# Performance work log

Hardware: AMD Instinct MI355X
Metric: run time of the kernel (lower is better)

## Reference

```python
import jax, jax.numpy as jnp
import numpy as np

B, L, D, H, NL, V, W = 4, 2048, 512, 8, 4, 258, 8
HD = D // H


def setup_inputs() -> dict:
    key = jax.random.key(0)
    ks = jax.random.split(key, 12)
    s = 0.02
    x = jax.random.randint(ks[0], (B, L), 0, V, dtype=jnp.int32)
    patch_lengths = jnp.full((B, 256), W, dtype=jnp.int32)  # sum over patches == L
    emb = jax.random.normal(ks[1], (V, D), jnp.float32) * s
    ent_w = jax.random.normal(ks[2], (D, 1), jnp.float32) * s
    ent_b = jnp.zeros((D,), jnp.float32)
    qkv_w = jax.random.normal(ks[3], (NL, 3 * D, D), jnp.float32) * s
    qkv_b = jnp.zeros((NL, 3 * D), jnp.float32)
    ao_w = jax.random.normal(ks[4], (NL, D, D), jnp.float32) * s
    ao_b = jnp.zeros((NL, D), jnp.float32)
    ln1_s = jnp.ones((NL, D), jnp.float32)
    ln1_b = jnp.zeros((NL, D), jnp.float32)
    ln2_s = jnp.ones((NL, D), jnp.float32)
    ln2_b = jnp.zeros((NL, D), jnp.float32)
    ff1_w = jax.random.normal(ks[5], (NL, 4 * D, D), jnp.float32) * s
    ff1_b = jnp.zeros((NL, 4 * D), jnp.float32)
    ff2_w = jax.random.normal(ks[6], (NL, D, 4 * D), jnp.float32) * s
    ff2_b = jnp.zeros((NL, D), jnp.float32)
    out_w = jax.random.normal(ks[7], (V, D), jnp.float32) * s
    return {"emb": emb, "ent_w": ent_w, "ent_b": ent_b, "qkv_w": qkv_w,
            "qkv_b": qkv_b, "ao_w": ao_w, "ao_b": ao_b, "ln1_s": ln1_s,
            "ln1_b": ln1_b, "ln2_s": ln2_s, "ln2_b": ln2_b, "ff1_w": ff1_w,
            "ff1_b": ff1_b, "ff2_w": ff2_w, "ff2_b": ff2_b, "out_w": out_w,
            "x": x, "patch_lengths": patch_lengths}


def _layernorm(h, scale, bias, eps=1e-5):
    mu = jnp.mean(h, axis=-1, keepdims=True)
    var = jnp.mean(jnp.square(h - mu), axis=-1, keepdims=True)
    return (h - mu) * jax.lax.rsqrt(var + eps) * scale + bias


def _entropy_features(x, dtype):
    # fused sliding-window histogram via one-hot cumsum (replaces per-window bincount loop)
    onehot = jax.nn.one_hot(x, 256, dtype=dtype)            # [B, L, 256]
    c = jnp.cumsum(onehot, axis=1)
    cpad = jnp.concatenate([jnp.zeros_like(c[:, :1]), c], axis=1)
    counts = cpad[:, W:] - cpad[:, :-W]                     # [B, L-W+1, 256]
    p = counts / W
    ent = -jnp.sum(p * jnp.log2(p + 1e-10), axis=-1)        # zero-count terms contribute exactly 0
    full = jnp.zeros(x.shape, dtype).at[:, :x.shape[1] - W + 1].set(ent)
    return full[..., None]                                  # [B, L, 1]


def _block(h, p):
    qkv_w, qkv_b, ao_w, ao_b, l1s, l1b, l2s, l2b, f1w, f1b, f2w, f2b = p
    g = _layernorm(h, l1s, l1b)
    qkv = g @ qkv_w.T + qkv_b                                # [B, L, 3D]
    q, k, v = jnp.split(qkv, 3, axis=-1)
    q = q.reshape(B, L, H, HD)
    k = k.reshape(B, L, H, HD)
    v = v.reshape(B, L, H, HD)
    scores = jnp.einsum('blhd,bmhd->bhlm', q, k) / np.sqrt(HD).astype(h.dtype)
    attn = jax.nn.softmax(scores, axis=-1)
    o = jnp.einsum('bhlm,bmhd->blhd', attn, v).reshape(B, L, D)
    h = h + o @ ao_w.T + ao_b
    g = _layernorm(h, l2s, l2b)
    g = jax.nn.gelu(g @ f1w.T + f1b, approximate=False) @ f2w.T + f2b
    return h + g, None


def reference(emb, ent_w, ent_b, qkv_w, qkv_b, ao_w, ao_b, ln1_s, ln1_b,
              ln2_s, ln2_b, ff1_w, ff1_b, ff2_w, ff2_b, out_w, x, patch_lengths):
    tok = emb[x]                                             # [B, L, D]
    ent = _entropy_features(x, tok.dtype)                    # [B, L, 1]
    ent_emb = ent * ent_w[:, 0] + ent_b                      # Linear(1, D)
    h = tok + ent_emb
    h, _ = jax.lax.scan(_block, h,
                        (qkv_w, qkv_b, ao_w, ao_b, ln1_s, ln1_b,
                         ln2_s, ln2_b, ff1_w, ff1_b, ff2_w, ff2_b))
    # NOTE: the original module's global_transformer/patch-pool branch does not
    # feed the returned logits (dead code); logits come from the local stream h.
    logits = h @ out_w.T                                     # [B, L, V]
    return logits
```

## Files before the change

### kernel.cpp

```cpp
#include <hip/hip_runtime.h>
#include <hip/hip_bf16.h>
#include <math.h>

#define BB 4
#define LL 2048
#define DD 512
#define HH 8
#define NLAYER 4
#define VV 258
#define WW 8
#define HDIM 64
#define MM (BB * LL)
#define VPAD 384

typedef __attribute__((ext_vector_type(8))) short short8v;
typedef __attribute__((ext_vector_type(4))) float float4v;

typedef __attribute__((address_space(3))) unsigned int lds_u32;
typedef const __attribute__((address_space(1))) unsigned int glb_u32;

__device__ __forceinline__ unsigned short f2bf(float x) {
    unsigned int u = __float_as_uint(x);
    unsigned int r = (u + 0x7fffu + ((u >> 16) & 1u)) >> 16;
    return (unsigned short)r;
}

__device__ __forceinline__ unsigned lds_addr(const void* p) {
    return (unsigned)(size_t)(__attribute__((address_space(3))) const void*)p;
}

__global__ __launch_bounds__(256)
void cvt_kernel(const float* __restrict__ in, unsigned short* __restrict__ out, int n)
{
    int i = (blockIdx.x * 256 + threadIdx.x) * 4;
    if (i < n) {
        float4 v = *reinterpret_cast<const float4*>(in + i);
        uint2 pk;
        pk.x = (unsigned)f2bf(v.x) | ((unsigned)f2bf(v.y) << 16);
        pk.y = (unsigned)f2bf(v.z) | ((unsigned)f2bf(v.w) << 16);
        *reinterpret_cast<uint2*>(out + i) = pk;
    }
}

__global__ __launch_bounds__(256)
void cvt_pad_kernel(const float* __restrict__ in, unsigned short* __restrict__ out)
{
    int i = blockIdx.x * 256 + threadIdx.x;
    int row = i >> 9;
    out[i] = (row < VV) ? f2bf(in[i]) : (unsigned short)0;
}

__global__ __launch_bounds__(256)
void embed_ent_kernel(const int* __restrict__ x,
                      const float* __restrict__ emb,
                      const float* __restrict__ ent_w,
                      const float* __restrict__ ent_b,
                      float* __restrict__ h)
{
    int row = blockIdx.x;
    int b = row / LL, l = row % LL;

    float ent = 0.f;
    if (l <= LL - WW) {
        int win[WW];
        #pragma unroll
        for (int i = 0; i < WW; i++) win[i] = x[b * LL + l + i];
        float s = 0.f;
        #pragma unroll
        for (int i = 0; i < WW; i++) {
            if (win[i] < 256) {
                int c = 0;
                #pragma unroll
                for (int j = 0; j < WW; j++) c += (win[j] == win[i]) ? 1 : 0;
                s += log2f((float)c * 0.125f + 1e-10f);
            }
        }
        ent = -s * 0.125f;
    }

    int tok = x[b * LL + l];
    const float* erow = emb + (size_t)tok * DD;
    float* hrow = h + (size_t)row * DD;
    for (int d = threadIdx.x; d < DD; d += blockDim.x) {
        hrow[d] = erow[d] + ent * ent_w[d] + ent_b[d];
    }
}

__global__ __launch_bounds__(256)
void ln_kernel(const float* __restrict__ h,
               const float* __restrict__ scale,
               const float* __restrict__ bias,
               unsigned short* __restrict__ g)
{
    int w = threadIdx.x >> 6, lane = threadIdx.x & 63;
    int row = blockIdx.x * 4 + w;
    const float* hr = h + (size_t)row * DD + lane * 8;

    float v[8];
    *reinterpret_cast<float4*>(v)     = *reinterpret_cast<const float4*>(hr);
    *reinterpret_cast<float4*>(v + 4) = *reinterpret_cast<const float4*>(hr + 4);

    float sum = 0.f, sq = 0.f;
    #pragma unroll
    for (int i = 0; i < 8; i++) { sum += v[i]; sq += v[i] * v[i]; }
    #pragma unroll
    for (int off = 32; off > 0; off >>= 1) {
        sum += __shfl_xor(sum, off);
        sq  += __shfl_xor(sq, off);
    }
    float mu = sum * (1.f / DD);
    float var = sq * (1.f / DD) - mu * mu;
    float rstd = rsqrtf(var + 1e-5f);

    float s[8], bi[8];
    *reinterpret_cast<float4*>(s)      = *reinterpret_cast<const float4*>(scale + lane * 8);
    *reinterpret_cast<float4*>(s + 4)  = *reinterpret_cast<const float4*>(scale + lane * 8 + 4);
    *reinterpret_cast<float4*>(bi)     = *reinterpret_cast<const float4*>(bias + lane * 8);
    *reinterpret_cast<float4*>(bi + 4) = *reinterpret_cast<const float4*>(bias + lane * 8 + 4);

    unsigned int pk[4];
    #pragma unroll
    for (int i = 0; i < 4; i++) {
        unsigned short lo = f2bf((v[2*i]   - mu) * rstd * s[2*i]   + bi[2*i]);
        unsigned short hi = f2bf((v[2*i+1] - mu) * rstd * s[2*i+1] + bi[2*i+1]);
        pk[i] = (unsigned)lo | ((unsigned)hi << 16);
    }
    *reinterpret_cast<uint4*>(g + (size_t)row * DD + lane * 8) =
        *reinterpret_cast<const uint4*>(pk);
}

template<bool HAS_BIAS, bool GELU, bool RESID, bool OUT_BF16>
__global__ __launch_bounds__(256)
void gemm_mfma(const unsigned short* __restrict__ A,
               const unsigned short* __restrict__ W,
               const float* __restrict__ bias,
               const float* __restrict__ resid,
               void* __restrict__ Cv,
               int Nn, int Kk)
{
    __shared__ unsigned short As[2][128 * 64];
    __shared__ unsigned short Bs[2][128 * 64];

    int t = threadIdx.x;
    int w = t >> 6, lane = t & 63;
    int wr = w >> 1, wc = w & 1;
    int l15 = lane & 15, l4 = lane >> 4;
    int m0 = blockIdx.y * 128, n0 = blockIdx.x * 128;

    int lrow = lane >> 3;
    int segp = (lane & 7) ^ lrow;

    float4v acc[4][4];
    #pragma unroll
    for (int i = 0; i < 4; i++)
        #pragma unroll
        for (int j = 0; j < 4; j++)
            acc[i][j] = (float4v){0.f, 0.f, 0.f, 0.f};

    #define STAGE(buf, k0) do {                                                   \
        _Pragma("unroll")                                                         \
        for (int i_ = 0; i_ < 4; i_++) {                                          \
            int r_ = i_ * 32 + w * 8 + lrow;                                      \
            __builtin_amdgcn_global_load_lds(                                     \
                (glb_u32*)(A + (size_t)(m0 + r_) * Kk + (k0) + segp * 8),         \
                (lds_u32*)(As[buf] + i_ * 2048 + w * 512), 16, 0, 0);             \
            __builtin_amdgcn_global_load_lds(                                     \
                (glb_u32*)(W + (size_t)(n0 + r_) * Kk + (k0) + segp * 8),         \
                (lds_u32*)(Bs[buf] + i_ * 2048 + w * 512), 16, 0, 0);             \
        } } while (0)

    int nk = Kk >> 6;
    STAGE(0, 0);
    for (int kt = 0; kt < nk; kt++) {
        int cur = kt & 1;
        if (kt + 1 < nk) {
            STAGE(cur ^ 1, (kt + 1) << 6);
            __builtin_amdgcn_sched_barrier(0);
            asm volatile("s_waitcnt vmcnt(8)");
            __builtin_amdgcn_sched_barrier(0);
        } else {
            __builtin_amdgcn_sched_barrier(0);
            asm volatile("s_waitcnt vmcnt(0)");
            __builtin_amdgcn_sched_barrier(0);
        }
        __builtin_amdgcn_s_barrier();

        const char* asb = (const char*)As[cur];
        const char* bsb = (const char*)Bs[cur];
        #pragma unroll
        for (int kc = 0; kc < 2; kc++) {
            short8v af[4], bfr[4];
            #pragma unroll
            for (int mf = 0; mf < 4; mf++) {
                int row = wr * 64 + mf * 16 + l15;
                int off = (row * 128 + kc * 64 + l4 * 16) ^ ((row & 7) << 4);
                af[mf] = *reinterpret_cast<const short8v*>(asb + off);
            }
            #pragma unroll
            for (int nf = 0; nf < 4; nf++) {
                int row = wc * 64 + nf * 16 + l15;
                int off = (row * 128 + kc * 64 + l4 * 16) ^ ((row & 7) << 4);
                bfr[nf] = *reinterpret_cast<const short8v*>(bsb + off);
            }
            #pragma unroll
            for (int mf = 0; mf < 4; mf++)
                #pragma unroll
                for (int nf = 0; nf < 4; nf++)
                    acc[mf][nf] = __builtin_amdgcn_mfma_f32_16x16x32_bf16(
                        af[mf], bfr[nf], acc[mf][nf], 0, 0, 0);
        }
        __builtin_amdgcn_s_barrier();
    }
    #undef STAGE

    #pragma unroll
    for (int mf = 0; mf < 4; mf++)
        #pragma unroll
        for (int nf = 0; nf < 4; nf++)
            #pragma unroll
            for (int r = 0; r < 4; r++) {
                int m = m0 + wr * 64 + mf * 16 + l4 * 4 + r;
                int n = n0 + wc * 64 + nf * 16 + l15;
                if (n < Nn) {
                    float v = acc[mf][nf][r];
                    if (HAS_BIAS) v += bias[n];
                    if (GELU)     v = 0.5f * v * (1.f + erff(v * 0.70710678118654752f));
                    if (RESID)    v += resid[(size_t)m * Nn + n];
                    if (OUT_BF16) ((unsigned short*)Cv)[(size_t)m * Nn + n] = f2bf(v);
                    else          ((float*)Cv)[(size_t)m * Nn + n] = v;
                }
            }
}

__global__ __launch_bounds__(512, 4)
void attn_mfma(const unsigned short* __restrict__ qkv, unsigned short* __restrict__ o)
{
    __shared__ unsigned short Kl[64 * 64];
    __shared__ unsigned short Vs[64 * 64];
    __shared__ unsigned short Pl[8 * 16 * 64];
    __shared__ float Scl[8][16];

    int t = threadIdx.x, w = t >> 6, lane = t & 63;
    int l15 = lane & 15, l4 = lane >> 4;

    int flat = blockIdx.x;
    int swz = (flat & 7) * 64 + (flat >> 3);
    int qt = swz & 15, hh = (swz >> 4) & 7, b = swz >> 7;

    int q0 = qt * 128 + w * 16;
    const int RS = 3 * DD;

    short8v qf[2];
    #pragma unroll
    for (int dh = 0; dh < 2; dh++) {
        size_t addr = (size_t)(b * LL + q0 + l15) * RS + hh * HDIM + dh * 32 + l4 * 8;
        qf[dh] = *reinterpret_cast<const short8v*>(qkv + addr);
    }

    float4v o_acc[4];
    #pragma unroll
    for (int dt = 0; dt < 4; dt++) o_acc[dt] = (float4v){0.f, 0.f, 0.f, 0.f};
    float m_run = -1e30f, l_run = 0.f;

    char* pbase = (char*)Pl + w * 2048;

    int krow = t >> 3, kseg = t & 7;
    int vrow = ((t >> 5) << 2) | ((t >> 1) & 3);
    int vseg = (((t >> 3) & 3) << 1) | (t & 1);

    unsigned vbase = lds_addr(Vs) + ((lane >> 4) << 10)
                   + (((lane >> 2) & 3) << 5) + ((lane & 3) << 3);

    for (int kb = 0; kb < LL / 64; kb++) {
        size_t gaK = (size_t)(b * LL + kb * 64 + krow) * RS + hh * HDIM + DD + kseg * 8;
        size_t gaV = (size_t)(b * LL + kb * 64 + vrow) * RS + hh * HDIM + 2 * DD + vseg * 8;
        short8v krg = *reinterpret_cast<const short8v*>(qkv + gaK);
        short8v vrg = *reinterpret_cast<const short8v*>(qkv + gaV);
        __syncthreads();
        {
            int koff = (krow * 128 + kseg * 16) ^ ((krow & 7) << 4);
            *reinterpret_cast<short8v*>((char*)Kl + koff) = krg;
            *reinterpret_cast<short8v*>((char*)Vs + t * 16) = vrg;
        }
        __syncthreads();

        float4v s_acc[4];
        __builtin_amdgcn_s_setprio(1);
        #pragma unroll
        for (int nt = 0; nt < 4; nt++) {
            s_acc[nt] = (float4v){0.f, 0.f, 0.f, 0.f};
            #pragma unroll
            for (int dh = 0; dh < 2; dh++) {
                int row = nt * 16 + l15;
                int off = (row * 128 + dh * 64 + l4 * 16) ^ ((row & 7) << 4);
                short8v kf = *reinterpret_cast<const short8v*>((const char*)Kl + off);
                s_acc[nt] = __builtin_amdgcn_mfma_f32_16x16x32_bf16(kf, qf[dh], s_acc[nt], 0, 0, 0);
            }
        }
        __builtin_amdgcn_s_setprio(0);

        float mm = -1e30f;
        #pragma unroll
        for (int nt = 0; nt < 4; nt++)
            #pragma unroll
            for (int r = 0; r < 4; r++)
                mm = fmaxf(mm, s_acc[nt][r]);
        mm *= 0.125f;
        mm = fmaxf(mm, __shfl_xor(mm, 16));
        mm = fmaxf(mm, __shfl_xor(mm, 32));

        if (!__all(mm <= m_run + 8.f)) {
            float mnew = fmaxf(m_run, mm);
            float sc = __expf(m_run - mnew);
            m_run = mnew;
            l_run *= sc;
            if (l4 == 0) Scl[w][l15] = sc;
            float4 scv = *reinterpret_cast<const float4*>(&Scl[w][l4 * 4]);
            #pragma unroll
            for (int dt = 0; dt < 4; dt++) {
                o_acc[dt][0] *= scv.x; o_acc[dt][1] *= scv.y;
                o_acc[dt][2] *= scv.z; o_acc[dt][3] *= scv.w;
            }
        }

        float ps = 0.f;
        #pragma unroll
        for (int nt = 0; nt < 4; nt++) {
            float p0 = __expf(fmaf(s_acc[nt][0], 0.125f, -m_run));
            float p1 = __expf(fmaf(s_acc[nt][1], 0.125f, -m_run));
            float p2 = __expf(fmaf(s_acc[nt][2], 0.125f, -m_run));
            float p3 = __expf(fmaf(s_acc[nt][3], 0.125f, -m_run));
            ps += (p0 + p1) + (p2 + p3);
            unsigned int pk0, pk1;
            asm("v_cvt_pk_bf16_f32 %0, %1, %2" : "=v"(pk0) : "v"(p0), "v"(p1));
            asm("v_cvt_pk_bf16_f32 %0, %1, %2" : "=v"(pk1) : "v"(p2), "v"(p3));
            uint2 pk; pk.x = pk0; pk.y = pk1;
            int off = (l15 * 128 + nt * 32 + l4 * 8) ^ ((l15 & 7) << 4);
            *reinterpret_cast<uint2*>(pbase + off) = pk;
        }
        l_run += ps;

        #pragma unroll
        for (int kc = 0; kc < 2; kc++) {
            int poff = (l15 * 128 + kc * 64 + l4 * 16) ^ ((l15 & 7) << 4);
            short8v pf = *reinterpret_cast<const short8v*>(pbase + poff);
            unsigned long long tr0, tr1, tr2, tr3, tr4, tr5, tr6, tr7;
            unsigned ab = vbase + kc * 4096;
            asm volatile("ds_read_b64_tr_b16 %0, %1" : "=v"(tr0) : "v"(ab));
            asm volatile("ds_read_b64_tr_b16 %0, %1" : "=v"(tr1) : "v"(ab + 512));
            asm volatile("ds_read_b64_tr_b16 %0, %1" : "=v"(tr2) : "v"(ab + 128));
            asm volatile("ds_read_b64_tr_b16 %0, %1" : "=v"(tr3) : "v"(ab + 640));
            asm volatile("ds_read_b64_tr_b16 %0, %1" : "=v"(tr4) : "v"(ab + 256));
            asm volatile("ds_read_b64_tr_b16 %0, %1" : "=v"(tr5) : "v"(ab + 768));
            asm volatile("ds_read_b64_tr_b16 %0, %1" : "=v"(tr6) : "v"(ab + 384));
            asm volatile("ds_read_b64_tr_b16 %0, %1" : "=v"(tr7) : "v"(ab + 896));
            asm volatile("s_waitcnt lgkmcnt(0)");
            __builtin_amdgcn_sched_barrier(0);
            __builtin_amdgcn_s_setprio(1);
            union { unsigned long long q[2]; short8v v; } u0, u1, u2, u3;
            u0.q[0] = tr0; u0.q[1] = tr1;
            u1.q[0] = tr2; u1.q[1] = tr3;
            u2.q[0] = tr4; u2.q[1] = tr5;
            u3.q[0] = tr6; u3.q[1] = tr7;
            o_acc[0] = __builtin_amdgcn_mfma_f32_16x16x32_bf16(pf, u0.v, o_acc[0], 0, 0, 0);
            o_acc[1] = __builtin_amdgcn_mfma_f32_16x16x32_bf16(pf, u1.v, o_acc[1], 0, 0, 0);
            o_acc[2] = __builtin_amdgcn_mfma_f32_16x16x32_bf16(pf, u2.v, o_acc[2], 0, 0, 0);
            o_acc[3] = __builtin_amdgcn_mfma_f32_16x16x32_bf16(pf, u3.v, o_acc[3], 0, 0, 0);
            __builtin_amdgcn_s_setprio(0);
        }
    }

    float lt = l_run;
    lt += __shfl_xor(lt, 16);
    lt += __shfl_xor(lt, 32);
    if (l4 == 0) Scl[w][l15] = 1.f / lt;
    float4 iv = *reinterpret_cast<const float4*>(&Scl[w][l4 * 4]);
    float invs[4] = {iv.x, iv.y, iv.z, iv.w};
    #pragma unroll
    for (int r = 0; r < 4; r++) {
        int qg = q0 + l4 * 4 + r;
        #pragma unroll
        for (int dt = 0; dt < 4; dt++) {
            o[(size_t)(b * LL + qg) * DD + hh * HDIM + dt * 16 + l15] =
                f2bf(o_acc[dt][r] * invs[r]);
        }
    }
}

extern "C" void kernel_launch(void* const* d_in, const int* in_sizes, int n_in,
                              void* d_out, int out_size, void* d_ws, size_t ws_size,
                              hipStream_t stream)
{
    const float* emb    = (const float*)d_in[0];
    const float* ent_w  = (const float*)d_in[1];
    const float* ent_b  = (const float*)d_in[2];
    const float* qkv_w  = (const float*)d_in[3];
    const float* qkv_b  = (const float*)d_in[4];
    const float* ao_w   = (const float*)d_in[5];
    const float* ao_b   = (const float*)d_in[6];
    const float* ln1_s  = (const float*)d_in[7];
    const float* ln1_b  = (const float*)d_in[8];
    const float* ln2_s  = (const float*)d_in[9];
    const float* ln2_b  = (const float*)d_in[10];
    const float* ff1_w  = (const float*)d_in[11];
    const float* ff1_b  = (const float*)d_in[12];
    const float* ff2_w  = (const float*)d_in[13];
    const float* ff2_b  = (const float*)d_in[14];
    const float* out_w  = (const float*)d_in[15];
    const int*   x      = (const int*)d_in[16];

    float* out = (float*)d_out;

    const int NQW = NLAYER * 3 * DD * DD;
    const int NAW = NLAYER * DD * DD;
    const int NF1 = NLAYER * 4 * DD * DD;
    const int NF2 = NLAYER * DD * 4 * DD;

    char* p = (char*)d_ws;
    unsigned short* wq  = (unsigned short*)p; p += (size_t)NQW * 2;
    unsigned short* wa  = (unsigned short*)p; p += (size_t)NAW * 2;
    unsigned short* w1  = (unsigned short*)p; p += (size_t)NF1 * 2;
    unsigned short* w2  = (unsigned short*)p; p += (size_t)NF2 * 2;
    unsigned short* wob = (unsigned short*)p; p += (size_t)VPAD * DD * 2;
    float*          h   = (float*)p;          p += (size_t)MM * DD * 4;
    unsigned short* hb  = (unsigned short*)p; p += (size_t)MM * DD * 2;
    unsigned short* gb  = (unsigned short*)p; p += (size_t)MM * DD * 2;
    unsigned short* ob  = (unsigned short*)p; p += (size_t)MM * DD * 2;
    unsigned short* bb  = (unsigned short*)p; p += (size_t)MM * 4 * DD * 2;

    dim3 blk(256);

    cvt_kernel<<<NQW / 1024, blk, 0, stream>>>(qkv_w, wq, NQW);
    cvt_kernel<<<NAW / 1024, blk, 0, stream>>>(ao_w,  wa, NAW);
    cvt_kernel<<<NF1 / 1024, blk, 0, stream>>>(ff1_w, w1, NF1);
    cvt_kernel<<<NF2 / 1024, blk, 0, stream>>>(ff2_w, w2, NF2);
    cvt_pad_kernel<<<(VPAD * DD) / 256, blk, 0, stream>>>(out_w, wob);

    embed_ent_kernel<<<MM, blk, 0, stream>>>(x, emb, ent_w, ent_b, h);

    for (int layer = 0; layer < NLAYER; layer++) {
        const unsigned short* qw = wq + (size_t)layer * 3 * DD * DD;
        const unsigned short* aw = wa + (size_t)layer * DD * DD;
        const unsigned short* f1 = w1 + (size_t)layer * 4 * DD * DD;
        const unsigned short* f2 = w2 + (size_t)layer * DD * 4 * DD;
        const float* qb  = qkv_b + (size_t)layer * 3 * DD;
        const float* ab  = ao_b  + (size_t)layer * DD;
        const float* l1s = ln1_s + (size_t)layer * DD;
        const float* l1b = ln1_b + (size_t)layer * DD;
        const float* l2s = ln2_s + (size_t)layer * DD;
        const float* l2b = ln2_b + (size_t)layer * DD;
        const float* f1b = ff1_b + (size_t)layer * 4 * DD;
        const float* f2b = ff2_b + (size_t)layer * DD;

        ln_kernel<<<MM / 4, blk, 0, stream>>>(h, l1s, l1b, gb);

        {
            dim3 grid((3 * DD) / 128, MM / 128);
            gemm_mfma<true, false, false, true><<<grid, blk, 0, stream>>>(
                gb, qw, qb, nullptr, bb, 3 * DD, DD);
        }

        attn_mfma<<<512, 512, 0, stream>>>(bb, ob);

        {
            dim3 grid(DD / 128, MM / 128);
            gemm_mfma<true, false, true, false><<<grid, blk, 0, stream>>>(
                ob, aw, ab, h, h, DD, DD);
        }

        ln_kernel<<<MM / 4, blk, 0, stream>>>(h, l2s, l2b, gb);

        {
            dim3 grid((4 * DD) / 128, MM / 128);
            gemm_mfma<true, true, false, true><<<grid, blk, 0, stream>>>(
                gb, f1, f1b, nullptr, bb, 4 * DD, DD);
        }

        {
            dim3 grid(DD / 128, MM / 128);
            gemm_mfma<true, false, true, false><<<grid, blk, 0, stream>>>(
                bb, f2, f2b, h, h, DD, 4 * DD);
        }
    }

    cvt_kernel<<<(MM * DD) / 1024, blk, 0, stream>>>(h, hb, MM * DD);
    {
        dim3 grid(VPAD / 128, MM / 128);
        gemm_mfma<false, false, false, false><<<grid, blk, 0, stream>>>(
            hb, wob, nullptr, nullptr, out, VV, DD);
    }
}
```

Baseline: 800.7 us.

## Double-buffer attention K/V tiles and fuse embed+LN and final bf16 cast

Attention now double-buffers K/V in LDS, prefetching the next tile into registers while computing on the current one. This leaves one barrier per iteration instead of two, and launch bounds drop to 2 blocks per SM to fit the extra LDS. The embedding kernel is fused with the first layernorm, and the last FF2 GEMM also writes a bf16 copy of h. Together these remove one LN launch and the final conversion pass, at the cost of lower occupancy in attention.

```diff
diff --git a/kernel.cpp b/kernel.cpp
--- a/kernel.cpp
+++ b/kernel.cpp
@@ -51,13 +51,17 @@
 }
 
 __global__ __launch_bounds__(256)
-void embed_ent_kernel(const int* __restrict__ x,
-                      const float* __restrict__ emb,
-                      const float* __restrict__ ent_w,
-                      const float* __restrict__ ent_b,
-                      float* __restrict__ h)
-{
-    int row = blockIdx.x;
+void embed_ln_kernel(const int* __restrict__ x,
+                     const float* __restrict__ emb,
+                     const float* __restrict__ ent_w,
+                     const float* __restrict__ ent_b,
+                     const float* __restrict__ ln_s,
+                     const float* __restrict__ ln_b,
+                     float* __restrict__ h,
+                     unsigned short* __restrict__ g)
+{
+    int w = threadIdx.x >> 6, lane = threadIdx.x & 63;
+    int row = blockIdx.x * 4 + w;
     int b = row / LL, l = row % LL;
 
     float ent = 0.f;
@@ -78,12 +82,50 @@
         ent = -s * 0.125f;
     }
 
-    int tok = x[b * LL + l];
-    const float* erow = emb + (size_t)tok * DD;
-    float* hrow = h + (size_t)row * DD;
-    for (int d = threadIdx.x; d < DD; d += blockDim.x) {
-        hrow[d] = erow[d] + ent * ent_w[d] + ent_b[d];
-    }
+    int tok = x[row];
+    const float* erow = emb + (size_t)tok * DD + lane * 8;
+    float v[8], ew[8], eb[8];
+    *reinterpret_cast<float4*>(v)      = *reinterpret_cast<const float4*>(erow);
+    *reinterpret_cast<float4*>(v + 4)  = *reinterpret_cast<const float4*>(erow + 4);
+    *reinterpret_cast<float4*>(ew)     = *reinterpret_cast<const float4*>(ent_w + lane * 8);
+    *reinterpret_cast<float4*>(ew + 4) = *reinterpret_cast<const float4*>(ent_w + lane * 8 + 4);
+    *reinterpret_cast<float4*>(eb)     = *reinterpret_cast<const float4*>(ent_b + lane * 8);
+    *reinterpret_cast<float4*>(eb + 4) = *reinterpret_cast<const float4*>(ent_b + lane * 8 + 4);
+
+    float sum = 0.f, sq = 0.f;
+    #pragma unroll
+    for (int i = 0; i < 8; i++) {
+        v[i] = v[i] + ent * ew[i] + eb[i];
+        sum += v[i]; sq += v[i] * v[i];
+    }
+    float* hr = h + (size_t)row * DD + lane * 8;
+    *reinterpret_cast<float4*>(hr)     = *reinterpret_cast<const float4*>(v);
+    *reinterpret_cast<float4*>(hr + 4) = *reinterpret_cast<const float4*>(v + 4);
+
+    #pragma unroll
+    for (int off = 32; off > 0; off >>= 1) {
+        sum += __shfl_xor(sum, off);
+        sq  += __shfl_xor(sq, off);
+    }
+    float mu = sum * (1.f / DD);
+    float var = sq * (1.f / DD) - mu * mu;
+    float rstd = rsqrtf(var + 1e-5f);
+
+    float s8[8], bi[8];
+    *reinterpret_cast<float4*>(s8)     = *reinterpret_cast<const float4*>(ln_s + lane * 8);
+    *reinterpret_cast<float4*>(s8 + 4) = *reinterpret_cast<const float4*>(ln_s + lane * 8 + 4);
+    *reinterpret_cast<float4*>(bi)     = *reinterpret_cast<const float4*>(ln_b + lane * 8);
+    *reinterpret_cast<float4*>(bi + 4) = *reinterpret_cast<const float4*>(ln_b + lane * 8 + 4);
+
+    unsigned int pk[4];
+    #pragma unroll
+    for (int i = 0; i < 4; i++) {
+        unsigned short lo = f2bf((v[2*i]   - mu) * rstd * s8[2*i]   + bi[2*i]);
+        unsigned short hi = f2bf((v[2*i+1] - mu) * rstd * s8[2*i+1] + bi[2*i+1]);
+        pk[i] = (unsigned)lo | ((unsigned)hi << 16);
+    }
+    *reinterpret_cast<uint4*>(g + (size_t)row * DD + lane * 8) =
+        *reinterpret_cast<const uint4*>(pk);
 }
 
 __global__ __launch_bounds__(256)
@@ -129,13 +171,14 @@
         *reinterpret_cast<const uint4*>(pk);
 }
 
-template<bool HAS_BIAS, bool GELU, bool RESID, bool OUT_BF16>
+template<bool HAS_BIAS, bool GELU, bool RESID, int OMODE>
 __global__ __launch_bounds__(256)
 void gemm_mfma(const unsigned short* __restrict__ A,
                const unsigned short* __restrict__ W,
                const float* __restrict__ bias,
                const float* __restrict__ resid,
                void* __restrict__ Cv,
+               unsigned short* __restrict__ Cb,
                int Nn, int Kk)
 {
     __shared__ unsigned short As[2][128 * 64];
@@ -226,17 +269,21 @@
                     if (HAS_BIAS) v += bias[n];
                     if (GELU)     v = 0.5f * v * (1.f + erff(v * 0.70710678118654752f));
                     if (RESID)    v += resid[(size_t)m * Nn + n];
-                    if (OUT_BF16) ((unsigned short*)Cv)[(size_t)m * Nn + n] = f2bf(v);
-                    else          ((float*)Cv)[(size_t)m * Nn + n] = v;
+                    if (OMODE == 1) {
+                        ((unsigned short*)Cv)[(size_t)m * Nn + n] = f2bf(v);
+                    } else {
+                        ((float*)Cv)[(size_t)m * Nn + n] = v;
+                        if (OMODE == 2) Cb[(size_t)m * Nn + n] = f2bf(v);
+                    }
                 }
             }
 }
 
-__global__ __launch_bounds__(512, 4)
+__global__ __launch_bounds__(512, 2)
 void attn_mfma(const unsigned short* __restrict__ qkv, unsigned short* __restrict__ o)
 {
-    __shared__ unsigned short Kl[64 * 64];
-    __shared__ unsigned short Vs[64 * 64];
+    __shared__ unsigned short Kl[2][64 * 64];
+    __shared__ unsigned short Vs[2][64 * 64];
     __shared__ unsigned short Pl[8 * 16 * 64];
     __shared__ float Scl[8][16];
 
@@ -267,22 +314,34 @@
     int krow = t >> 3, kseg = t & 7;
     int vrow = ((t >> 5) << 2) | ((t >> 1) & 3);
     int vseg = (((t >> 3) & 3) << 1) | (t & 1);
-
-    unsigned vbase = lds_addr(Vs) + ((lane >> 4) << 10)
-                   + (((lane >> 2) & 3) << 5) + ((lane & 3) << 3);
+    int koff = (krow * 128 + kseg * 16) ^ ((krow & 7) << 4);
+    int voff = t * 16;
+
+    const unsigned short* kptr = qkv + (size_t)(b * LL + krow) * RS + hh * HDIM + DD + kseg * 8;
+    const unsigned short* vptr = qkv + (size_t)(b * LL + vrow) * RS + hh * HDIM + 2 * DD + vseg * 8;
+    const int step = 64 * RS;
+
+    unsigned vtrbase = lds_addr(Vs) + ((lane >> 4) << 10)
+                     + (((lane >> 2) & 3) << 5) + ((lane & 3) << 3);
+
+    {
+        short8v krg = *reinterpret_cast<const short8v*>(kptr); kptr += step;
+        short8v vrg = *reinterpret_cast<const short8v*>(vptr); vptr += step;
+        *reinterpret_cast<short8v*>((char*)Kl[0] + koff) = krg;
+        *reinterpret_cast<short8v*>((char*)Vs[0] + voff) = vrg;
+    }
+    __syncthreads();
 
     for (int kb = 0; kb < LL / 64; kb++) {
-        size_t gaK = (size_t)(b * LL + kb * 64 + krow) * RS + hh * HDIM + DD + kseg * 8;
-        size_t gaV = (size_t)(b * LL + kb * 64 + vrow) * RS + hh * HDIM + 2 * DD + vseg * 8;
-        short8v krg = *reinterpret_cast<const short8v*>(qkv + gaK);
-        short8v vrg = *reinterpret_cast<const short8v*>(qkv + gaV);
-        __syncthreads();
-        {
-            int koff = (krow * 128 + kseg * 16) ^ ((krow & 7) << 4);
-            *reinterpret_cast<short8v*>((char*)Kl + koff) = krg;
-            *reinterpret_cast<short8v*>((char*)Vs + t * 16) = vrg;
-        }
-        __syncthreads();
+        int cur = kb & 1;
+        short8v krg, vrg;
+        if (kb + 1 < LL / 64) {
+            krg = *reinterpret_cast<const short8v*>(kptr); kptr += step;
+            vrg = *reinterpret_cast<const short8v*>(vptr); vptr += step;
+        }
+
+        const char* klc = (const char*)Kl[cur];
+        unsigned vb = vtrbase + cur * 8192;
 
         float4v s_acc[4];
         __builtin_amdgcn_s_setprio(1);
@@ -293,7 +352,7 @@
             for (int dh = 0; dh < 2; dh++) {
                 int row = nt * 16 + l15;
                 int off = (row * 128 + dh * 64 + l4 * 16) ^ ((row & 7) << 4);
-                short8v kf = *reinterpret_cast<const short8v*>((const char*)Kl + off);
+                short8v kf = *reinterpret_cast<const short8v*>(klc + off);
                 s_acc[nt] = __builtin_amdgcn_mfma_f32_16x16x32_bf16(kf, qf[dh], s_acc[nt], 0, 0, 0);
             }
         }
@@ -345,7 +404,7 @@
             int poff = (l15 * 128 + kc * 64 + l4 * 16) ^ ((l15 & 7) << 4);
             short8v pf = *reinterpret_cast<const short8v*>(pbase + poff);
             unsigned long long tr0, tr1, tr2, tr3, tr4, tr5, tr6, tr7;
-            unsigned ab = vbase + kc * 4096;
+            unsigned ab = vb + kc * 4096;
             asm volatile("ds_read_b64_tr_b16 %0, %1" : "=v"(tr0) : "v"(ab));
             asm volatile("ds_read_b64_tr_b16 %0, %1" : "=v"(tr1) : "v"(ab + 512));
             asm volatile("ds_read_b64_tr_b16 %0, %1" : "=v"(tr2) : "v"(ab + 128));
@@ -368,6 +427,12 @@
             o_acc[3] = __builtin_amdgcn_mfma_f32_16x16x32_bf16(pf, u3.v, o_acc[3], 0, 0, 0);
             __builtin_amdgcn_s_setprio(0);
         }
+
+        if (kb + 1 < LL / 64) {
+            *reinterpret_cast<short8v*>((char*)Kl[cur ^ 1] + koff) = krg;
+            *reinterpret_cast<short8v*>((char*)Vs[cur ^ 1] + voff) = vrg;
+        }
+        __syncthreads();
     }
 
     float lt = l_run;
@@ -436,7 +501,8 @@
     cvt_kernel<<<NF2 / 1024, blk, 0, stream>>>(ff2_w, w2, NF2);
     cvt_pad_kernel<<<(VPAD * DD) / 256, blk, 0, stream>>>(out_w, wob);
 
-    embed_ent_kernel<<<MM, blk, 0, stream>>>(x, emb, ent_w, ent_b, h);
+    embed_ln_kernel<<<MM / 4, blk, 0, stream>>>(x, emb, ent_w, ent_b,
+                                                ln1_s, ln1_b, h, gb);
 
     for (int layer = 0; layer < NLAYER; layer++) {
         const unsigned short* qw = wq + (size_t)layer * 3 * DD * DD;
@@ -452,41 +518,45 @@
         const float* f1b = ff1_b + (size_t)layer * 4 * DD;
         const float* f2b = ff2_b + (size_t)layer * DD;
 
-        ln_kernel<<<MM / 4, blk, 0, stream>>>(h, l1s, l1b, gb);
+        if (layer > 0)
+            ln_kernel<<<MM / 4, blk, 0, stream>>>(h, l1s, l1b, gb);
 
         {
             dim3 grid((3 * DD) / 128, MM / 128);
-            gemm_mfma<true, false, false, true><<<grid, blk, 0, stream>>>(
-                gb, qw, qb, nullptr, bb, 3 * DD, DD);
+            gemm_mfma<true, false, false, 1><<<grid, blk, 0, stream>>>(
+                gb, qw, qb, nullptr, bb, nullptr, 3 * DD, DD);
         }
 
         attn_mfma<<<512, 512, 0, stream>>>(bb, ob);
 
         {
             dim3 grid(DD / 128, MM / 128);
-            gemm_mfma<true, false, true, false><<<grid, blk, 0, stream>>>(
-                ob, aw, ab, h, h, DD, DD);
+            gemm_mfma<true, false, true, 0><<<grid, blk, 0, stream>>>(
+                ob, aw, ab, h, h, nullptr, DD, DD);
         }
 
         ln_kernel<<<MM / 4, blk, 0, stream>>>(h, l2s, l2b, gb);
 
         {
             dim3 grid((4 * DD) / 128, MM / 128);
-            gemm_mfma<true, true, false, true><<<grid, blk, 0, stream>>>(
-                gb, f1, f1b, nullptr, bb, 4 * DD, DD);
+            gemm_mfma<true, true, false, 1><<<grid, blk, 0, stream>>>(
+                gb, f1, f1b, nullptr, bb, nullptr, 4 * DD, DD);
         }
 
         {
             dim3 grid(DD / 128, MM / 128);
-            gemm_mfma<true, false, true, false><<<grid, blk, 0, stream>>>(
-                bb, f2, f2b, h, h, DD, 4 * DD);
-        }
-    }
-
-    cvt_kernel<<<(MM * DD) / 1024, blk, 0, stream>>>(h, hb, MM * DD);
+            if (layer == NLAYER - 1)
+                gemm_mfma<true, false, true, 2><<<grid, blk, 0, stream>>>(
+                    bb, f2, f2b, h, h, hb, DD, 4 * DD);
+            else
+                gemm_mfma<true, false, true, 0><<<grid, blk, 0, stream>>>(
+                    bb, f2, f2b, h, h, nullptr, DD, 4 * DD);
+        }
+    }
+
     {
         dim3 grid(VPAD / 128, MM / 128);
-        gemm_mfma<false, false, false, false><<<grid, blk, 0, stream>>>(
-            hb, wob, nullptr, nullptr, out, VV, DD);
-    }
-}
+        gemm_mfma<false, false, false, 0><<<grid, blk, 0, stream>>>(
+            hb, wob, nullptr, nullptr, out, nullptr, VV, DD);
+    }
+}
```

Measured after the change: 782.2 us. -2.3%, faster.
